# Kernel optimization log

Measured on AMD Instinct MI355X. Metric: run time of the kernel, lower is better.

The kernel has to match this reference:

```python
import jax, jax.numpy as jnp
import numpy as np

B, S, D, H, F = 4, 1024, 1024, 16, 4096
DH = D // H
EPS = 1e-3  # keras LayerNormalization default epsilon


def _layer_norm(x, g, b):
    mu = jnp.mean(x, axis=-1, keepdims=True)
    var = jnp.mean(jnp.square(x - mu), axis=-1, keepdims=True)
    return (x - mu) * jax.lax.rsqrt(var + EPS) * g + b


def setup_inputs() -> dict:
    key = jax.random.key(0)
    ks = jax.random.split(key, 12)
    p = lambda k, shape: (0.02 * jax.random.normal(k, shape, dtype=jnp.float32))
    inp = {
        "inputs": jax.random.normal(ks[0], (B, S, D), dtype=jnp.float32),
        "paddings": jnp.zeros((B, S), dtype=jnp.float32),
        "attention_bias": jax.random.normal(ks[1], (B, H, S, S), dtype=jnp.float32),
        "attention_mask": jnp.ones((B, S, S), dtype=jnp.float32),
        "ln1_g": jnp.ones((D,), jnp.float32), "ln1_b": jnp.zeros((D,), jnp.float32),
        "wq": p(ks[2], (D, D)), "bq": jnp.zeros((D,), jnp.float32),
        "wk": p(ks[3], (D, D)), "bk": jnp.zeros((D,), jnp.float32),
        "wv": p(ks[4], (D, D)), "bv": jnp.zeros((D,), jnp.float32),
        "wo": p(ks[5], (D, D)), "bo": jnp.zeros((D,), jnp.float32),
        "ln2_g": jnp.ones((D,), jnp.float32), "ln2_b": jnp.zeros((D,), jnp.float32),
        "w1": p(ks[6], (D, F)), "b1": jnp.zeros((F,), jnp.float32),
        "w2": p(ks[7], (F, D)), "b2": jnp.zeros((D,), jnp.float32),
    }
    return inp


def reference(inputs, paddings, attention_bias, attention_mask,
              ln1_g, ln1_b, wq, bq, wk, bk, wv, bv, wo, bo,
              ln2_g, ln2_b, w1, b1, w2, b2):
    # ----- combined mask: [B,S,S] (broadcast over heads) -----
    keep = 1.0 - paddings                           # [B,S]
    pad_mask = keep[:, :, None] * keep[:, None, :]  # [B,T,S]
    mask = attention_mask * pad_mask                # [B,T,S]

    # ----- self-attention on pre-normalized inputs -----
    xn = _layer_norm(inputs, ln1_g, ln1_b)          # [B,S,D]
    q = (xn @ wq + bq).reshape(B, S, H, DH)
    k = (xn @ wk + bk).reshape(B, S, H, DH)
    v = (xn @ wv + bv).reshape(B, S, H, DH)

    logits = jnp.einsum('bthd,bshd->bhts', q, k) / jnp.sqrt(jnp.float32(DH))
    logits = logits + attention_bias - 1e9 * (1.0 - mask[:, None, :, :])
    attn = jax.nn.softmax(logits, axis=-1)          # [B,H,T,S]
    ctx = jnp.einsum('bhts,bshd->bthd', attn, v).reshape(B, S, D)
    atten_out = ctx @ wo + bo + inputs              # residual

    # ----- feed-forward block -----
    yn = _layer_norm(atten_out, ln2_g, ln2_b)
    h = jax.nn.gelu(yn @ w1 + b1, approximate=False)  # keras 'gelu' is exact
    out = atten_out + (h @ w2 + b2)
    out = out * (1.0 - paddings[:, :, None])
    return out
```

## Files before the change

kernel.cpp:

```cpp
#include <hip/hip_runtime.h>
#include <cstdint>
#include <cstddef>

#define B_   4
#define S_   1024
#define D_   1024
#define H_   16
#define DH_  64
#define F_   4096
#define MTOT 4096
#define QKV3 3072
#define KOFF 1024
#define VOFF 2048
#define SMBASE 16.0f

typedef __bf16 bf16x8 __attribute__((ext_vector_type(8)));
typedef float  f32x4  __attribute__((ext_vector_type(4)));

__device__ __forceinline__ unsigned short f2bf(float f){
  uint32_t u = __builtin_bit_cast(uint32_t, f);
  u += 0x7fffu + ((u >> 16) & 1u);
  return (unsigned short)(u >> 16);
}

__device__ __forceinline__ void gload_lds16(const void* g, void* l){
  __builtin_amdgcn_global_load_lds((__attribute__((address_space(1))) void*)(g),
                                   (__attribute__((address_space(3))) void*)(l),
                                   16, 0, 0);
}

__global__ __launch_bounds__(256) void prep_weights(const float* __restrict__ wq,
                                                    const float* __restrict__ wk,
                                                    const float* __restrict__ wv,
                                                    const float* __restrict__ wo,
                                                    const float* __restrict__ w1,
                                                    const float* __restrict__ w2,
                                                    const float* __restrict__ bq,
                                                    const float* __restrict__ bk,
                                                    const float* __restrict__ bv,
                                                    unsigned short* __restrict__ wqkvT,
                                                    unsigned short* __restrict__ woT,
                                                    unsigned short* __restrict__ w1T,
                                                    unsigned short* __restrict__ w2T,
                                                    float* __restrict__ bqkv){
  __shared__ float tile[32][33];
  const int bid = blockIdx.x;
  const int tx = threadIdx.x, ty = threadIdx.y;
  const float* W; unsigned short* WT; int K, N, n0, k0;
  if (bid < 3072){
    W  = (bid < 1024) ? wq : (bid < 2048) ? wk : wv;
    WT = wqkvT + (size_t)(bid >> 10) * D_ * D_;
    K = D_; N = D_;
    const int t = bid & 1023; n0 = (t & 31) * 32; k0 = (t >> 5) * 32;
  } else if (bid < 4096){
    W = wo; WT = woT; K = D_; N = D_;
    const int t = bid - 3072; n0 = (t & 31) * 32; k0 = (t >> 5) * 32;
  } else if (bid < 8192){
    W = w1; WT = w1T; K = D_; N = F_;
    const int t = bid - 4096; n0 = (t & 127) * 32; k0 = (t >> 7) * 32;
  } else {
    W = w2; WT = w2T; K = F_; N = D_;
    const int t = bid - 8192; n0 = (t & 31) * 32; k0 = (t >> 5) * 32;
  }
  #pragma unroll
  for (int i = 0; i < 4; ++i)
    tile[ty + i*8][tx] = W[(size_t)(k0 + ty + i*8) * N + n0 + tx];
  __syncthreads();
  #pragma unroll
  for (int i = 0; i < 4; ++i)
    WT[(size_t)(n0 + ty + i*8) * K + k0 + tx] = f2bf(tile[tx][ty + i*8]);
  if (bid < 12){
    const int i = bid*256 + ty*32 + tx;
    bqkv[i] = (i < 1024) ? bq[i] : (i < 2048) ? bk[i - 1024] : bv[i - 2048];
  }
}

__global__ __launch_bounds__(256) void mid_prep(const unsigned short* __restrict__ qkv,
                                                unsigned short* __restrict__ vt,
                                                const float* __restrict__ amask,
                                                const float* __restrict__ pad,
                                                float* __restrict__ madd){
  const int bid = blockIdx.x;
  if (bid < 4096){
    __shared__ unsigned short tile[32][33];
    const int tx = threadIdx.x, ty = threadIdx.y;
    const int s0 = (bid & 31) * 32;
    const int d0 = ((bid >> 5) & 1) * 32;
    const int bh = bid >> 6;
    const int b = bh >> 4, hh = bh & 15;
    #pragma unroll
    for (int i = 0; i < 4; ++i)
      tile[ty + i*8][tx] = qkv[(size_t)(b*S_ + s0 + ty + i*8) * QKV3 + VOFF + hh*DH_ + d0 + tx];
    __syncthreads();
    #pragma unroll
    for (int i = 0; i < 4; ++i)
      vt[((size_t)bh*DH_ + d0 + ty + i*8) * S_ + s0 + tx] = tile[tx][ty + i*8];
  } else {
    const int tid = threadIdx.y*32 + threadIdx.x;
    const int total = B_ * S_ * S_ / 4;
    for (int idx = (bid - 4096)*256 + tid; idx < total; idx += 2048*256){
      const int e0 = idx * 4;
      const int b = e0 >> 20;
      const int t = (e0 >> 10) & (S_ - 1);
      const int s = e0 & (S_ - 1);
      const float kt = 1.0f - pad[b*S_ + t];
      const float4 m = *(const float4*)(amask + e0);
      float4 o;
      o.x = -1e9f * (1.0f - m.x * kt * (1.0f - pad[b*S_ + s + 0]));
      o.y = -1e9f * (1.0f - m.y * kt * (1.0f - pad[b*S_ + s + 1]));
      o.z = -1e9f * (1.0f - m.z * kt * (1.0f - pad[b*S_ + s + 2]));
      o.w = -1e9f * (1.0f - m.w * kt * (1.0f - pad[b*S_ + s + 3]));
      *(float4*)(madd + e0) = o;
    }
  }
}

__global__ __launch_bounds__(256) void ln_kernel(const float* __restrict__ x,
                                                 const float* __restrict__ g,
                                                 const float* __restrict__ b,
                                                 unsigned short* __restrict__ out){
  const int row = blockIdx.x;
  const int tid = threadIdx.x;
  float4 xv = ((const float4*)(x + (size_t)row * D_))[tid];
  float s  = xv.x + xv.y + xv.z + xv.w;
  float s2 = xv.x*xv.x + xv.y*xv.y + xv.z*xv.z + xv.w*xv.w;
  #pragma unroll
  for (int off = 32; off > 0; off >>= 1){
    s  += __shfl_down(s, off);
    s2 += __shfl_down(s2, off);
  }
  __shared__ float ws1[4], ws2[4];
  const int w = tid >> 6, lane = tid & 63;
  if (lane == 0){ ws1[w] = s; ws2[w] = s2; }
  __syncthreads();
  const float tot  = ws1[0] + ws1[1] + ws1[2] + ws1[3];
  const float tot2 = ws2[0] + ws2[1] + ws2[2] + ws2[3];
  const float mean = tot * (1.0f / D_);
  const float var  = tot2 * (1.0f / D_) - mean * mean;
  const float rstd = rsqrtf(var + 1e-3f);
  const int c0 = tid * 4;
  ushort4 o;
  o.x = f2bf((xv.x - mean) * rstd * g[c0+0] + b[c0+0]);
  o.y = f2bf((xv.y - mean) * rstd * g[c0+1] + b[c0+1]);
  o.z = f2bf((xv.z - mean) * rstd * g[c0+2] + b[c0+2]);
  o.w = f2bf((xv.w - mean) * rstd * g[c0+3] + b[c0+3]);
  *(ushort4*)(out + (size_t)row * D_ + c0) = o;
}

template<int EPI, int BM>
__global__ __launch_bounds__(256) void gemm_bt(const unsigned short* __restrict__ A,
                                               const unsigned short* __restrict__ BT,
                                               const float* __restrict__ bias,
                                               const float* __restrict__ resid,
                                               const float* __restrict__ pad,
                                               unsigned short* __restrict__ outB,
                                               float* __restrict__ outF,
                                               int N, int K){
  constexpr int MR = BM / 32;
  constexpr int RA = BM / 32;
  __shared__ unsigned short As[BM * 64];
  __shared__ unsigned short Bs[128 * 64];
  const int tid  = threadIdx.x;
  const int lane = tid & 63, w = tid >> 6;
  const int wr = w >> 1, wc = w & 1;
  const int lm = lane & 15, l4 = lane >> 4;
  const int xsw = (lm & 7) << 3;
  const int m0 = blockIdx.x * BM, n0 = blockIdx.y * 128;

  const int rrow = tid >> 3;
  const int ce   = (((tid & 7) ^ (rrow & 7)) << 3);
  const unsigned short* Asrc = A  + (size_t)(m0 + rrow) * K + ce;
  const unsigned short* Bsrc = BT + (size_t)(n0 + rrow) * K + ce;

  f32x4 acc[MR][4] = {};

  #pragma unroll
  for (int ra = 0; ra < RA; ++ra)
    gload_lds16(Asrc + (size_t)(ra*32) * K, &As[(ra*256 + w*64) * 8]);
  #pragma unroll
  for (int rb = 0; rb < 4; ++rb)
    gload_lds16(Bsrc + (size_t)(rb*32) * K, &Bs[(rb*256 + w*64) * 8]);

  for (int k0 = 0; k0 < K; k0 += 64){
    __syncthreads();

    bf16x8 a[MR][2], bb[4][2];
    #pragma unroll
    for (int m = 0; m < MR; ++m)
      #pragma unroll
      for (int kc = 0; kc < 2; ++kc)
        a[m][kc] = *(const bf16x8*)&As[(wr*(BM/2) + m*16 + lm)*64 + ((kc*32 + l4*8) ^ xsw)];
    #pragma unroll
    for (int n = 0; n < 4; ++n)
      #pragma unroll
      for (int kc = 0; kc < 2; ++kc)
        bb[n][kc] = *(const bf16x8*)&Bs[(wc*64 + n*16 + lm)*64 + ((kc*32 + l4*8) ^ xsw)];

    __syncthreads();

    if (k0 + 64 < K){
      #pragma unroll
      for (int ra = 0; ra < RA; ++ra)
        gload_lds16(Asrc + (size_t)(ra*32) * K + (k0 + 64), &As[(ra*256 + w*64) * 8]);
      #pragma unroll
      for (int rb = 0; rb < 4; ++rb)
        gload_lds16(Bsrc + (size_t)(rb*32) * K + (k0 + 64), &Bs[(rb*256 + w*64) * 8]);
    }

    #pragma unroll
    for (int m = 0; m < MR; ++m)
      #pragma unroll
      for (int n = 0; n < 4; ++n)
        #pragma unroll
        for (int kc = 0; kc < 2; ++kc)
          acc[m][n] = __builtin_amdgcn_mfma_f32_16x16x32_bf16(a[m][kc], bb[n][kc], acc[m][n], 0, 0, 0);
  }

  #pragma unroll
  for (int m = 0; m < MR; ++m){
    #pragma unroll
    for (int n = 0; n < 4; ++n){
      #pragma unroll
      for (int r = 0; r < 4; ++r){
        const int row = m0 + wr*(BM/2) + m*16 + l4*4 + r;
        const int col = n0 + wc*64 + n*16 + lm;
        const size_t idx = (size_t)row * N + col;
        float vv = acc[m][n][r] + bias[col];
        if constexpr (EPI == 0){
          outB[idx] = f2bf(vv);
        } else if constexpr (EPI == 1){
          outF[idx] = vv + resid[idx];
        } else if constexpr (EPI == 2){
          outB[idx] = f2bf(0.5f * vv * (1.0f + erff(vv * 0.70710678118654752f)));
        } else {
          float t = vv + resid[idx];
          outF[idx] = t * (1.0f - pad[row]);
        }
      }
    }
  }
}

__global__ __launch_bounds__(256) void attn_kernel(const unsigned short* __restrict__ qkv,
                                                   const unsigned short* __restrict__ vt,
                                                   const float* __restrict__ abias,
                                                   const float* __restrict__ madd,
                                                   unsigned short* __restrict__ ctx){
  const int bid = blockIdx.x;
  const int id2 = (bid & 7) * 128 + (bid >> 3);
  const int tt = id2 & 15, h = (id2 >> 4) & 15, b = id2 >> 8;
  const int t0 = tt * 64;
  const int tid = threadIdx.x;
  const int lane = tid & 63, w = tid >> 6;
  const int lm = lane & 15, l4 = lane >> 4;
  const int xsw = (lm & 7) << 3;

  __shared__ unsigned short Ks[2][64 * 64];
  __shared__ unsigned short VTs[2][64 * 64];
  __shared__ unsigned short Ps[4][16 * 64];

  bf16x8 aq[2];
  {
    const int tg = t0 + w*16 + lm;
    const size_t qb = (size_t)(b*S_ + tg) * QKV3 + h*DH_;
    aq[0] = *(const bf16x8*)&qkv[qb + 0  + l4*8];
    aq[1] = *(const bf16x8*)&qkv[qb + 32 + l4*8];
  }

  const unsigned short* kbase = qkv + (size_t)(b*S_) * QKV3 + KOFF + h*DH_;
  const unsigned short* vbase = vt  + (size_t)((b*H_ + h) * DH_) * S_;
  const float* biasbase = abias + (size_t)((b*H_ + h) * S_ + t0 + w*16 + l4*4) * S_;
  const float* maddbase = madd  + (size_t)(b*S_ + t0 + w*16 + l4*4) * S_;

  const int r_st  = tid >> 3;
  const int ce_st = (((tid & 7) ^ (r_st & 7)) << 3);
  const unsigned short* kst = kbase + (size_t)r_st * QKV3 + ce_st;
  const unsigned short* vst = vbase + (size_t)r_st * S_ + ce_st;

  f32x4 accO[4] = {};
  float lrow[4] = {};
  float bmA[4][4], bmB[4][4];

  gload_lds16(kst,                   &Ks[0][w*512]);
  gload_lds16(kst + (size_t)32*QKV3, &Ks[0][2048 + w*512]);
  gload_lds16(vst,                   &VTs[0][w*512]);
  gload_lds16(vst + 32*S_,           &VTs[0][2048 + w*512]);
  #pragma unroll
  for (int n = 0; n < 4; ++n){
    const int sg = n*16 + lm;
    #pragma unroll
    for (int r = 0; r < 4; ++r)
      bmA[n][r] = biasbase[(size_t)r * S_ + sg] + maddbase[(size_t)r * S_ + sg];
  }

  auto step = [&](int s0, int buf, float (&cur)[4][4], float (&nxt)[4][4]){
    __syncthreads();

    const int s1 = s0 + 64;
    if (s1 < S_){
      gload_lds16(kst + (size_t)s1*QKV3,        &Ks[buf^1][w*512]);
      gload_lds16(kst + (size_t)(s1 + 32)*QKV3, &Ks[buf^1][2048 + w*512]);
      gload_lds16(vst + s1,                     &VTs[buf^1][w*512]);
      gload_lds16(vst + 32*S_ + s1,             &VTs[buf^1][2048 + w*512]);
      #pragma unroll
      for (int n = 0; n < 4; ++n){
        const int sg = s1 + n*16 + lm;
        #pragma unroll
        for (int r = 0; r < 4; ++r)
          nxt[n][r] = biasbase[(size_t)r * S_ + sg] + maddbase[(size_t)r * S_ + sg];
      }
    }

    f32x4 accS[4] = {};
    __builtin_amdgcn_s_setprio(1);
    #pragma unroll
    for (int n = 0; n < 4; ++n)
      #pragma unroll
      for (int kc = 0; kc < 2; ++kc){
        bf16x8 bk_ = *(const bf16x8*)&Ks[buf][(n*16 + lm)*64 + ((kc*32 + l4*8) ^ xsw)];
        accS[n] = __builtin_amdgcn_mfma_f32_16x16x32_bf16(aq[kc], bk_, accS[n], 0, 0, 0);
      }
    __builtin_amdgcn_s_setprio(0);

    float ps[4] = {};
    #pragma unroll
    for (int n = 0; n < 4; ++n){
      #pragma unroll
      for (int r = 0; r < 4; ++r){
        const float pv = __expf(fmaf(accS[n][r], 0.125f, cur[n][r]) - SMBASE);
        accS[n][r] = pv;
        ps[r] += pv;
      }
    }
    #pragma unroll
    for (int r = 0; r < 4; ++r){
      float s = ps[r];
      s += __shfl_xor(s, 1); s += __shfl_xor(s, 2);
      s += __shfl_xor(s, 4); s += __shfl_xor(s, 8);
      lrow[r] += s;
    }

    #pragma unroll
    for (int n = 0; n < 4; ++n)
      #pragma unroll
      for (int r = 0; r < 4; ++r){
        const int prow = l4*4 + r;
        Ps[w][prow*64 + ((n*16 + lm) ^ ((prow & 7) << 3))] = f2bf(accS[n][r]);
      }

    __builtin_amdgcn_s_setprio(1);
    #pragma unroll
    for (int ks = 0; ks < 2; ++ks){
      bf16x8 ap = *(const bf16x8*)&Ps[w][lm*64 + ((ks*32 + l4*8) ^ xsw)];
      #pragma unroll
      for (int n = 0; n < 4; ++n){
        bf16x8 bv_ = *(const bf16x8*)&VTs[buf][(n*16 + lm)*64 + ((ks*32 + l4*8) ^ xsw)];
        accO[n] = __builtin_amdgcn_mfma_f32_16x16x32_bf16(ap, bv_, accO[n], 0, 0, 0);
      }
    }
    __builtin_amdgcn_s_setprio(0);
  };

  #pragma unroll 1
  for (int s0 = 0; s0 < S_; s0 += 128){
    step(s0,      0, bmA, bmB);
    step(s0 + 64, 1, bmB, bmA);
  }

  #pragma unroll
  for (int n = 0; n < 4; ++n)
    #pragma unroll
    for (int r = 0; r < 4; ++r){
      const int tg = t0 + w*16 + l4*4 + r;
      ctx[(size_t)(b*S_ + tg) * D_ + h*DH_ + n*16 + lm] = f2bf(accO[n][r] / lrow[r]);
    }
}

extern "C" void kernel_launch(void* const* d_in, const int* in_sizes, int n_in,
                              void* d_out, int out_size, void* d_ws, size_t ws_size,
                              hipStream_t stream){
  (void)in_sizes; (void)n_in; (void)out_size; (void)ws_size;
  const float* x     = (const float*)d_in[0];
  const float* pad   = (const float*)d_in[1];
  const float* abias = (const float*)d_in[2];
  const float* amask = (const float*)d_in[3];
  const float* ln1g  = (const float*)d_in[4];
  const float* ln1b  = (const float*)d_in[5];
  const float* wq    = (const float*)d_in[6];
  const float* bq    = (const float*)d_in[7];
  const float* wk    = (const float*)d_in[8];
  const float* bk    = (const float*)d_in[9];
  const float* wv    = (const float*)d_in[10];
  const float* bv    = (const float*)d_in[11];
  const float* wo    = (const float*)d_in[12];
  const float* bo    = (const float*)d_in[13];
  const float* ln2g  = (const float*)d_in[14];
  const float* ln2b  = (const float*)d_in[15];
  const float* w1    = (const float*)d_in[16];
  const float* b1    = (const float*)d_in[17];
  const float* w2    = (const float*)d_in[18];
  const float* b2    = (const float*)d_in[19];
  float* out = (float*)d_out;

  char* p = (char*)d_ws;
  auto take = [&](size_t bytes){ void* r = (void*)p; p += bytes; return r; };
  unsigned short* xn   = (unsigned short*)take((size_t)MTOT * D_ * 2);
  unsigned short* qkv  = (unsigned short*)take((size_t)MTOT * QKV3 * 2);
  unsigned short* ctx  = (unsigned short*)take((size_t)MTOT * D_ * 2);
  unsigned short* yn   = (unsigned short*)take((size_t)MTOT * D_ * 2);
  unsigned short* hb   = (unsigned short*)take((size_t)MTOT * F_ * 2);
  float*          ao   = (float*)take((size_t)MTOT * D_ * 4);
  unsigned short* wqkvT= (unsigned short*)take((size_t)QKV3 * D_ * 2);
  unsigned short* woT  = (unsigned short*)take((size_t)D_ * D_ * 2);
  unsigned short* w1T  = (unsigned short*)take((size_t)D_ * F_ * 2);
  unsigned short* w2T  = (unsigned short*)take((size_t)D_ * F_ * 2);
  float*          bqkv = (float*)take((size_t)QKV3 * 4);
  unsigned short* vtb  = xn;
  float*          madd = (float*)hb;

  const dim3 tb(32, 8);

  prep_weights<<<12288, tb, 0, stream>>>(wq, wk, wv, wo, w1, w2, bq, bk, bv,
                                         wqkvT, woT, w1T, w2T, bqkv);

  ln_kernel<<<MTOT, 256, 0, stream>>>(x, ln1g, ln1b, xn);

  gemm_bt<0,128><<<dim3(MTOT/128, QKV3/128), 256, 0, stream>>>(xn, wqkvT, bqkv, nullptr, nullptr, qkv, nullptr, QKV3, D_);

  mid_prep<<<6144, tb, 0, stream>>>(qkv, vtb, amask, pad, madd);

  attn_kernel<<<dim3(16*H_*B_), 256, 0, stream>>>(qkv, vtb, abias, madd, ctx);

  gemm_bt<1,64><<<dim3(MTOT/64, D_/128), 256, 0, stream>>>(ctx, woT, bo, x, nullptr, nullptr, ao, D_, D_);

  ln_kernel<<<MTOT, 256, 0, stream>>>(ao, ln2g, ln2b, yn);

  gemm_bt<2,128><<<dim3(MTOT/128, F_/128), 256, 0, stream>>>(yn, w1T, b1, nullptr, nullptr, hb, nullptr, F_, D_);

  gemm_bt<3,64><<<dim3(MTOT/64, D_/128), 256, 0, stream>>>(hb, w2T, b2, ao, pad, nullptr, out, D_, F_);
}
```

Measured before the change: 309.8 us.

## Fuse mask construction into attention and stage bias tiles through LDS

Removes the separate pass that materialised a [B,S,S] additive mask, and instead rebuilds the mask inside the attention kernel from attention_mask and paddings. The attention bias is now staged into shared memory with async global-to-LDS loads using a swizzled layout, and double-buffered like K and V. This avoids writing and re-reading 16MB of mask, at the cost of 32KB more LDS per block, which may lower occupancy, plus some extra per-element ALU work.

```diff
diff --git a/kernel.cpp b/kernel.cpp
--- a/kernel.cpp
+++ b/kernel.cpp
@@ -75,44 +75,22 @@
   }
 }
 
-__global__ __launch_bounds__(256) void mid_prep(const unsigned short* __restrict__ qkv,
-                                                unsigned short* __restrict__ vt,
-                                                const float* __restrict__ amask,
-                                                const float* __restrict__ pad,
-                                                float* __restrict__ madd){
+__global__ __launch_bounds__(256) void vtrans(const unsigned short* __restrict__ qkv,
+                                              unsigned short* __restrict__ vt){
+  __shared__ unsigned short tile[32][33];
+  const int tx = threadIdx.x, ty = threadIdx.y;
   const int bid = blockIdx.x;
-  if (bid < 4096){
-    __shared__ unsigned short tile[32][33];
-    const int tx = threadIdx.x, ty = threadIdx.y;
-    const int s0 = (bid & 31) * 32;
-    const int d0 = ((bid >> 5) & 1) * 32;
-    const int bh = bid >> 6;
-    const int b = bh >> 4, hh = bh & 15;
-    #pragma unroll
-    for (int i = 0; i < 4; ++i)
-      tile[ty + i*8][tx] = qkv[(size_t)(b*S_ + s0 + ty + i*8) * QKV3 + VOFF + hh*DH_ + d0 + tx];
-    __syncthreads();
-    #pragma unroll
-    for (int i = 0; i < 4; ++i)
-      vt[((size_t)bh*DH_ + d0 + ty + i*8) * S_ + s0 + tx] = tile[tx][ty + i*8];
-  } else {
-    const int tid = threadIdx.y*32 + threadIdx.x;
-    const int total = B_ * S_ * S_ / 4;
-    for (int idx = (bid - 4096)*256 + tid; idx < total; idx += 2048*256){
-      const int e0 = idx * 4;
-      const int b = e0 >> 20;
-      const int t = (e0 >> 10) & (S_ - 1);
-      const int s = e0 & (S_ - 1);
-      const float kt = 1.0f - pad[b*S_ + t];
-      const float4 m = *(const float4*)(amask + e0);
-      float4 o;
-      o.x = -1e9f * (1.0f - m.x * kt * (1.0f - pad[b*S_ + s + 0]));
-      o.y = -1e9f * (1.0f - m.y * kt * (1.0f - pad[b*S_ + s + 1]));
-      o.z = -1e9f * (1.0f - m.z * kt * (1.0f - pad[b*S_ + s + 2]));
-      o.w = -1e9f * (1.0f - m.w * kt * (1.0f - pad[b*S_ + s + 3]));
-      *(float4*)(madd + e0) = o;
-    }
-  }
+  const int s0 = (bid & 31) * 32;
+  const int d0 = ((bid >> 5) & 1) * 32;
+  const int bh = bid >> 6;
+  const int b = bh >> 4, hh = bh & 15;
+  #pragma unroll
+  for (int i = 0; i < 4; ++i)
+    tile[ty + i*8][tx] = qkv[(size_t)(b*S_ + s0 + ty + i*8) * QKV3 + VOFF + hh*DH_ + d0 + tx];
+  __syncthreads();
+  #pragma unroll
+  for (int i = 0; i < 4; ++i)
+    vt[((size_t)bh*DH_ + d0 + ty + i*8) * S_ + s0 + tx] = tile[tx][ty + i*8];
 }
 
 __global__ __launch_bounds__(256) void ln_kernel(const float* __restrict__ x,
@@ -244,7 +222,8 @@
 __global__ __launch_bounds__(256) void attn_kernel(const unsigned short* __restrict__ qkv,
                                                    const unsigned short* __restrict__ vt,
                                                    const float* __restrict__ abias,
-                                                   const float* __restrict__ madd,
+                                                   const float* __restrict__ amask,
+                                                   const float* __restrict__ pad,
                                                    unsigned short* __restrict__ ctx){
   const int bid = blockIdx.x;
   const int id2 = (bid & 7) * 128 + (bid >> 3);
@@ -257,6 +236,7 @@
 
   __shared__ unsigned short Ks[2][64 * 64];
   __shared__ unsigned short VTs[2][64 * 64];
+  __shared__ float          Bls[2][64 * 64];
   __shared__ unsigned short Ps[4][16 * 64];
 
   bf16x8 aq[2];
@@ -269,28 +249,50 @@
 
   const unsigned short* kbase = qkv + (size_t)(b*S_) * QKV3 + KOFF + h*DH_;
   const unsigned short* vbase = vt  + (size_t)((b*H_ + h) * DH_) * S_;
-  const float* biasbase = abias + (size_t)((b*H_ + h) * S_ + t0 + w*16 + l4*4) * S_;
-  const float* maddbase = madd  + (size_t)(b*S_ + t0 + w*16 + l4*4) * S_;
+  const float* biasT = abias + (size_t)((b*H_ + h) * S_ + t0) * S_;
+  const float* amaskbase = amask + (size_t)(b*S_ + t0 + w*16 + l4*4) * S_;
+  const float* padb = pad + b*S_;
 
   const int r_st  = tid >> 3;
   const int ce_st = (((tid & 7) ^ (r_st & 7)) << 3);
   const unsigned short* kst = kbase + (size_t)r_st * QKV3 + ce_st;
   const unsigned short* vst = vbase + (size_t)r_st * S_ + ce_st;
 
+  const int brow = lane >> 4;
+  const int bchk = lane & 15;
+
+  float kt[4];
+  #pragma unroll
+  for (int r = 0; r < 4; ++r)
+    kt[r] = 1.0f - padb[t0 + w*16 + l4*4 + r];
+
   f32x4 accO[4] = {};
   float lrow[4] = {};
-  float bmA[4][4], bmB[4][4];
-
-  gload_lds16(kst,                   &Ks[0][w*512]);
-  gload_lds16(kst + (size_t)32*QKV3, &Ks[0][2048 + w*512]);
-  gload_lds16(vst,                   &VTs[0][w*512]);
-  gload_lds16(vst + 32*S_,           &VTs[0][2048 + w*512]);
+  float mmA[4][4], mmB[4][4];
+
+  auto stageKV = [&](int s0, int buf){
+    gload_lds16(kst + (size_t)s0*QKV3,        &Ks[buf][w*512]);
+    gload_lds16(kst + (size_t)(s0 + 32)*QKV3, &Ks[buf][2048 + w*512]);
+    gload_lds16(vst + s0,                     &VTs[buf][w*512]);
+    gload_lds16(vst + 32*S_ + s0,             &VTs[buf][2048 + w*512]);
+  };
+  auto stageBias = [&](int s0, int buf){
+    #pragma unroll
+    for (int i = 0; i < 4; ++i){
+      const int row = (i*4 + w)*4 + brow;
+      const int csw = (bchk ^ (((row >> 2) & 3) << 2)) << 2;
+      gload_lds16(biasT + (size_t)row * S_ + s0 + csw, &Bls[buf][(i*4 + w)*256]);
+    }
+  };
+
+  stageKV(0, 0);
+  stageBias(0, 0);
   #pragma unroll
   for (int n = 0; n < 4; ++n){
     const int sg = n*16 + lm;
     #pragma unroll
     for (int r = 0; r < 4; ++r)
-      bmA[n][r] = biasbase[(size_t)r * S_ + sg] + maddbase[(size_t)r * S_ + sg];
+      mmA[n][r] = amaskbase[(size_t)r * S_ + sg];
   }
 
   auto step = [&](int s0, int buf, float (&cur)[4][4], float (&nxt)[4][4]){
@@ -298,16 +300,14 @@
 
     const int s1 = s0 + 64;
     if (s1 < S_){
-      gload_lds16(kst + (size_t)s1*QKV3,        &Ks[buf^1][w*512]);
-      gload_lds16(kst + (size_t)(s1 + 32)*QKV3, &Ks[buf^1][2048 + w*512]);
-      gload_lds16(vst + s1,                     &VTs[buf^1][w*512]);
-      gload_lds16(vst + 32*S_ + s1,             &VTs[buf^1][2048 + w*512]);
+      stageKV(s1, buf^1);
+      stageBias(s1, buf^1);
       #pragma unroll
       for (int n = 0; n < 4; ++n){
         const int sg = s1 + n*16 + lm;
         #pragma unroll
         for (int r = 0; r < 4; ++r)
-          nxt[n][r] = biasbase[(size_t)r * S_ + sg] + maddbase[(size_t)r * S_ + sg];
+          nxt[n][r] = amaskbase[(size_t)r * S_ + sg];
       }
     }
 
@@ -322,12 +322,22 @@
       }
     __builtin_amdgcn_s_setprio(0);
 
+    float ksv[4];
+    #pragma unroll
+    for (int n = 0; n < 4; ++n)
+      ksv[n] = 1.0f - padb[s0 + n*16 + lm];
+
     float ps[4] = {};
     #pragma unroll
     for (int n = 0; n < 4; ++n){
+      const int e = n*16 + lm;
       #pragma unroll
       for (int r = 0; r < 4; ++r){
-        const float pv = __expf(fmaf(accS[n][r], 0.125f, cur[n][r]) - SMBASE);
+        const int lrw = w*16 + l4*4 + r;
+        const float bb = Bls[buf][lrw*64 + (e ^ (((lrw >> 2) & 3) << 4))];
+        const float mm = cur[n][r] * kt[r] * ksv[n];
+        const float ma = -1e9f * (1.0f - mm);
+        const float pv = __expf(fmaf(accS[n][r], 0.125f, bb + ma) - SMBASE);
         accS[n][r] = pv;
         ps[r] += pv;
       }
@@ -363,8 +373,8 @@
 
   #pragma unroll 1
   for (int s0 = 0; s0 < S_; s0 += 128){
-    step(s0,      0, bmA, bmB);
-    step(s0 + 64, 1, bmB, bmA);
+    step(s0,      0, mmA, mmB);
+    step(s0 + 64, 1, mmB, mmA);
   }
 
   #pragma unroll
@@ -416,7 +426,6 @@
   unsigned short* w2T  = (unsigned short*)take((size_t)D_ * F_ * 2);
   float*          bqkv = (float*)take((size_t)QKV3 * 4);
   unsigned short* vtb  = xn;
-  float*          madd = (float*)hb;
 
   const dim3 tb(32, 8);
 
@@ -427,9 +436,9 @@
 
   gemm_bt<0,128><<<dim3(MTOT/128, QKV3/128), 256, 0, stream>>>(xn, wqkvT, bqkv, nullptr, nullptr, qkv, nullptr, QKV3, D_);
 
-  mid_prep<<<6144, tb, 0, stream>>>(qkv, vtb, amask, pad, madd);
-
-  attn_kernel<<<dim3(16*H_*B_), 256, 0, stream>>>(qkv, vtb, abias, madd, ctx);
+  vtrans<<<4096, tb, 0, stream>>>(qkv, vtb);
+
+  attn_kernel<<<dim3(16*H_*B_), 256, 0, stream>>>(qkv, vtb, abias, amask, pad, ctx);
 
   gemm_bt<1,64><<<dim3(MTOT/64, D_/128), 256, 0, stream>>>(ctx, woT, bo, x, nullptr, nullptr, ao, D_, D_);
 
```

Result: slower. 316.2 us (+2.1%).
